# Optimization experiments

Hardware: AMD Instinct MI355X
Metric: run time of the kernel (lower is better)

The kernel has to match this reference:

```python
import jax, jax.numpy as jnp
import numpy as np

OUTLINER_RATIO = 0.01
SUB_OUTLINER_BIT = 8
NEG_INF = -1e9


def setup_inputs() -> dict:
    key = jax.random.key(0)
    T, H, D = 4096, 8, 64
    qkv = jax.random.normal(key, (T, 3, H, D), dtype=jnp.float32)
    cu_seqlens = jnp.array([0, 1024, 2048, 3072, 4096], dtype=jnp.int32)
    return {"qkv": qkv, "cu_seqlens": cu_seqlens, "max_seqlen": 1024}


def _varlen_attention(q, k, v, cu_seqlens, causal=False):
    # q,k,v: [T, H, D]; sequences delimited by cu_seqlens (attention never
    # crosses segment boundaries, matching flash_attn_varlen semantics).
    T, H, D = q.shape
    scale = D ** (-0.5)
    pos = jnp.arange(T)
    seg = jnp.searchsorted(cu_seqlens, pos, side="right") - 1  # [T] segment ids
    mask = seg[:, None] == seg[None, :]                          # [T, T]
    if causal:
        mask = mask & (pos[:, None] >= pos[None, :])
    scores = jnp.einsum("thd,shd->hts", q, k) * scale            # [H, T, T]
    scores = jnp.where(mask[None, :, :], scores, NEG_INF)
    probs = jax.nn.softmax(scores, axis=-1)
    out = jnp.einsum("hts,shd->thd", probs, v)                   # [T, H, D]
    return out


def _outlier_quant_compress(x, outliner_ratio=OUTLINER_RATIO, bit=SUB_OUTLINER_BIT):
    # Outlier detection: keep top-ratio |x| entries in full precision;
    # quantize the residual (sub-outliers) to `bit` bits per-tensor.
    a = jnp.abs(x)
    thr = jnp.quantile(a.reshape(-1), 1.0 - outliner_ratio)
    outliers = jnp.where(a > thr, x, 0.0)
    resid = x - outliers
    qmax = 2.0 ** (bit - 1) - 1.0
    scale = jnp.maximum(jnp.max(jnp.abs(resid)), 1e-8) / qmax
    q = jnp.clip(jnp.round(resid / scale), -qmax, qmax)
    x_hat = outliers + q * scale  # decompressed approximation
    return x_hat, thr, scale


def reference(qkv, cu_seqlens, max_seqlen):
    q, k, v = qkv[:, 0], qkv[:, 1], qkv[:, 2]
    out = _varlen_attention(q, k, v, cu_seqlens, causal=False)
    # Compression pipeline (stats + quantize) runs on Q,K,V,O in the original
    # forward; it does not alter the forward output.
    for t in (q, k, v, out):
        _outlier_quant_compress(t)
    return out
```

## Files before the change

### kernel.cpp

```cpp
#include <hip/hip_runtime.h>


#define HEADS 8
#define DH 64
#define TQ 64
#define TK 64
#define PSTR 72
#define NEG_BIG -1e30f
#define L2E 1.44269504088896340736f

using f32x4 = __attribute__((ext_vector_type(4))) float;
using s16x8 = __attribute__((ext_vector_type(8))) short;

__device__ inline unsigned short bf16b(float x) {
    union { float f; unsigned u; } c; c.f = x;
    unsigned r = c.u + 0x7fffu + ((c.u >> 16) & 1u);
    return (unsigned short)(r >> 16);
}

#if __has_builtin(__builtin_amdgcn_cvt_pk_bf16_f32)
__device__ inline unsigned pk2(float a, float b) {
    auto v = __builtin_amdgcn_cvt_pk_bf16_f32(a, b);
    unsigned u; __builtin_memcpy(&u, &v, 4); return u;
}
#else
__device__ inline unsigned pk2(float a, float b) {
    return (unsigned)bf16b(a) | ((unsigned)bf16b(b) << 16);
}
#endif

__global__ __launch_bounds__(256)
void prep_kernel(const float* __restrict__ qkv, unsigned short* __restrict__ Qb,
                 unsigned short* __restrict__ Kb, unsigned short* __restrict__ Vtb,
                 int T) {
    __shared__ unsigned short Lt[64][PSTR];
    const int m = blockIdx.z, h = blockIdx.y, t0 = blockIdx.x * 64;
    const int tid = threadIdx.x, d8 = tid & 7, tr = tid >> 3;

    #pragma unroll
    for (int i = 0; i < 2; ++i) {
        int t = t0 + i * 32 + tr;
        int tc = t < T ? t : T - 1;
        const float* src = qkv + ((size_t)tc * 3 + m) * (HEADS * DH) + h * DH + d8 * 8;
        float4 a = *(const float4*)src;
        float4 b = *(const float4*)(src + 4);
        if (m == 0) {
            a.x *= 0.125f; a.y *= 0.125f; a.z *= 0.125f; a.w *= 0.125f;
            b.x *= 0.125f; b.y *= 0.125f; b.z *= 0.125f; b.w *= 0.125f;
        }
        unsigned p0 = pk2(a.x, a.y), p1 = pk2(a.z, a.w);
        unsigned p2 = pk2(b.x, b.y), p3 = pk2(b.z, b.w);
        if (m == 2) {
            *(uint2*)&Lt[i * 32 + tr][d8 * 8]     = make_uint2(p0, p1);
            *(uint2*)&Lt[i * 32 + tr][d8 * 8 + 4] = make_uint2(p2, p3);
        } else if (t < T) {
            unsigned short* dst = (m == 0)
                ? (Qb + (size_t)t * (HEADS * DH) + h * DH + d8 * 8)
                : (Kb + ((size_t)h * T + t) * DH + d8 * 8);
            *(uint4*)dst = make_uint4(p0, p1, p2, p3);
        }
    }
    if (m == 2) {
        __syncthreads();
        const int d = tid >> 2, tg = tid & 3;
        #pragma unroll
        for (int p = 0; p < 2; ++p) {
            int G = tg + 4 * p;
            int td = t0 + G * 8;
            unsigned u[4];
            #pragma unroll
            for (int jj = 0; jj < 4; ++jj)
                u[jj] = (unsigned)Lt[G * 8 + 2 * jj][d] |
                        ((unsigned)Lt[G * 8 + 2 * jj + 1][d] << 16);
            if (td < T)
                *(uint4*)(Vtb + ((size_t)h * DH + d) * T + td) =
                    make_uint4(u[0], u[1], u[2], u[3]);
        }
    }
}

__global__ __launch_bounds__(256, 4)
void fa_main(const unsigned short* __restrict__ Qb, const unsigned short* __restrict__ Kb,
             const unsigned short* __restrict__ Vtb, const int* __restrict__ cu,
             int n_cu, int T, float* __restrict__ out,
             float* __restrict__ Opart, float* __restrict__ Mp, float* __restrict__ Lp) {
    __shared__ unsigned short Ksh[TK * DH];
    __shared__ unsigned short Vsh[DH * TK];
    __shared__ unsigned short Psh[TQ][PSTR];

    const int tid = threadIdx.x;
    const int h = blockIdx.y, t0 = blockIdx.x * TQ;
    const int split = blockIdx.z, nsplit = gridDim.z;
    const int w = tid >> 6, lane = tid & 63, n15 = lane & 15, quad = lane >> 4;

    int trow = t0 + w * 16 + n15; if (trow > T - 1) trow = T - 1;
    int lo, hi;
    { int s = 0; for (int j = 1; j < n_cu - 1; ++j) if (cu[j] <= trow) s = j;
      lo = cu[s]; hi = cu[s + 1]; }
    int kb_, ke;
    { int s = 0; for (int j = 1; j < n_cu - 1; ++j) if (cu[j] <= t0) s = j;
      kb_ = cu[s];
      int tl = t0 + TQ - 1; if (tl > T - 1) tl = T - 1;
      s = 0; for (int j = 1; j < n_cu - 1; ++j) if (cu[j] <= tl) s = j;
      ke = cu[s + 1]; }

    s16x8 qfrag[2];
    {
        int tc = t0 + w * 16 + n15; if (tc > T - 1) tc = T - 1;
        const unsigned short* qp = Qb + (size_t)tc * (HEADS * DH) + h * DH + quad * 8;
        qfrag[0] = *(const s16x8*)qp;
        qfrag[1] = *(const s16x8*)(qp + 32);
    }

    const unsigned short* kb_h = Kb + (size_t)h * T * DH;
    const unsigned short* vt_h = Vtb + (size_t)h * DH * T;
    int krow_rel[2], vkey_off[2];
    const unsigned short* kbase[2];
    const unsigned short* vbase[2];
    #pragma unroll
    for (int i = 0; i < 2; ++i) {
        int gg = i * 64 + lane;
        int rr = gg >> 3;
        int gc = gg & 7;
        int row = w * 16 + rr;
        int gcol = gc ^ (row & 7);
        krow_rel[i] = row;
        kbase[i] = kb_h + gcol * 8;
        vbase[i] = vt_h + (size_t)row * T;
        vkey_off[i] = gcol * 8;
    }
    int off16[2];
    #pragma unroll
    for (int kh = 0; kh < 2; ++kh)
        off16[kh] = n15 * 128 + (((kh * 4 + quad) ^ (n15 & 7)) * 16);

    f32x4 oacc[4];
    #pragma unroll
    for (int i = 0; i < 4; ++i) oacc[i] = (f32x4){0.f, 0.f, 0.f, 0.f};
    float m_ = NEG_BIG, l_ = 0.f;

    const int c0_start = (kb_ / TK) * TK + split * TK;
    for (int c0 = c0_start; c0 < ke; c0 += nsplit * TK) {
        #pragma unroll
        for (int i = 0; i < 2; ++i) {
            int rk = c0 + krow_rel[i]; if (rk > T - 1) rk = T - 1;
            __builtin_amdgcn_global_load_lds(
                (const __attribute__((address_space(1))) void*)(kbase[i] + ((size_t)rk << 6)),
                (__attribute__((address_space(3))) void*)&Ksh[(w * 128 + i * 64) * 8],
                16, 0, 0);
            int kv = c0 + vkey_off[i]; if (kv > T - 8) kv = T - 8;
            __builtin_amdgcn_global_load_lds(
                (const __attribute__((address_space(1))) void*)(vbase[i] + kv),
                (__attribute__((address_space(3))) void*)&Vsh[(w * 128 + i * 64) * 8],
                16, 0, 0);
        }
        __syncthreads();

        const char* Kc = (const char*)Ksh;
        f32x4 sacc[4];
        #pragma unroll
        for (int nt = 0; nt < 4; ++nt) {
            s16x8 k0 = *(const s16x8*)(Kc + nt * 2048 + off16[0]);
            s16x8 k1 = *(const s16x8*)(Kc + nt * 2048 + off16[1]);
            f32x4 z = (f32x4){0.f, 0.f, 0.f, 0.f};
            z = __builtin_amdgcn_mfma_f32_16x16x32_bf16(k0, qfrag[0], z, 0, 0, 0);
            z = __builtin_amdgcn_mfma_f32_16x16x32_bf16(k1, qfrag[1], z, 0, 0, 0);
            sacc[nt] = z;
        }

        if (!(c0 >= lo && c0 + TK <= hi)) {
            #pragma unroll
            for (int nt = 0; nt < 4; ++nt)
                #pragma unroll
                for (int reg = 0; reg < 4; ++reg) {
                    int key = c0 + nt * 16 + quad * 4 + reg;
                    bool valid = (key >= lo) && (key < hi);
                    sacc[nt][reg] = valid ? sacc[nt][reg] : NEG_BIG;
                }
        }

        float rm = NEG_BIG;
        #pragma unroll
        for (int nt = 0; nt < 4; ++nt)
            #pragma unroll
            for (int reg = 0; reg < 4; ++reg) rm = fmaxf(rm, sacc[nt][reg]);
        rm = fmaxf(rm, __shfl_xor(rm, 16));
        rm = fmaxf(rm, __shfl_xor(rm, 32));
        float mn = fmaxf(m_, rm);
        float alpha = exp2f((m_ - mn) * L2E);
        float mnl = mn * L2E;
        float rs = 0.f;
        #pragma unroll
        for (int nt = 0; nt < 4; ++nt) {
            float p0 = exp2f(fmaf(sacc[nt][0], L2E, -mnl));
            float p1 = exp2f(fmaf(sacc[nt][1], L2E, -mnl));
            float p2 = exp2f(fmaf(sacc[nt][2], L2E, -mnl));
            float p3 = exp2f(fmaf(sacc[nt][3], L2E, -mnl));
            rs += (p0 + p1) + (p2 + p3);
            *(uint2*)&Psh[w * 16 + n15][nt * 16 + quad * 4] =
                make_uint2(pk2(p0, p1), pk2(p2, p3));
        }
        rs += __shfl_xor(rs, 16);
        rs += __shfl_xor(rs, 32);
        l_ = fmaf(l_, alpha, rs);
        m_ = mn;
        #pragma unroll
        for (int reg = 0; reg < 4; ++reg) {
            float ar = __shfl(alpha, quad * 4 + reg);
            oacc[0][reg] *= ar; oacc[1][reg] *= ar;
            oacc[2][reg] *= ar; oacc[3][reg] *= ar;
        }

        s16x8 afr[2];
        afr[0] = *(const s16x8*)&Psh[w * 16 + n15][quad * 8];
        afr[1] = *(const s16x8*)&Psh[w * 16 + n15][32 + quad * 8];
        const char* Vc = (const char*)Vsh;
        #pragma unroll
        for (int nt = 0; nt < 4; ++nt) {
            s16x8 v0 = *(const s16x8*)(Vc + nt * 2048 + off16[0]);
            s16x8 v1 = *(const s16x8*)(Vc + nt * 2048 + off16[1]);
            oacc[nt] = __builtin_amdgcn_mfma_f32_16x16x32_bf16(afr[0], v0, oacc[nt], 0, 0, 0);
            oacc[nt] = __builtin_amdgcn_mfma_f32_16x16x32_bf16(afr[1], v1, oacc[nt], 0, 0, 0);
        }
        __syncthreads();
    }

    if (nsplit == 1) {
        #pragma unroll
        for (int reg = 0; reg < 4; ++reg) {
            float lr = __shfl(l_, quad * 4 + reg);
            float inv = 1.f / fmaxf(lr, 1e-30f);
            int t = t0 + w * 16 + quad * 4 + reg;
            if (t < T) {
                #pragma unroll
                for (int nt = 0; nt < 4; ++nt)
                    out[((size_t)t * HEADS + h) * DH + nt * 16 + n15] = oacc[nt][reg] * inv;
            }
        }
    } else {
        #pragma unroll
        for (int reg = 0; reg < 4; ++reg) {
            int t = t0 + w * 16 + quad * 4 + reg;
            if (t < T) {
                size_t base = (((size_t)split * T + t) * HEADS + h) * DH;
                #pragma unroll
                for (int nt = 0; nt < 4; ++nt)
                    Opart[base + nt * 16 + n15] = oacc[nt][reg];
            }
        }
        int tq = t0 + w * 16 + n15;
        if (quad == 0 && tq < T) {
            size_t mi = ((size_t)split * T + tq) * HEADS + h;
            Mp[mi] = m_; Lp[mi] = l_;
        }
    }
}

__global__ __launch_bounds__(256)
void fa_combine_kernel(const float* __restrict__ Opart, const float* __restrict__ Mp,
                       const float* __restrict__ Lp, float* __restrict__ out, int T) {
    int i4 = blockIdx.x * blockDim.x + threadIdx.x;
    int total = T * HEADS * (DH / 4);
    if (i4 >= total) return;
    int th = i4 / (DH / 4);
    int d4 = i4 - th * (DH / 4);
    size_t stride = (size_t)T * HEADS * DH;
    int mlstride = T * HEADS;
    float m0 = Mp[th], m1 = Mp[mlstride + th];
    float l0 = Lp[th], l1 = Lp[mlstride + th];
    float M = fmaxf(m0, m1);
    float w0 = exp2f((m0 - M) * L2E);
    float w1 = exp2f((m1 - M) * L2E);
    float L = fmaxf(fmaf(l0, w0, l1 * w1), 1e-30f);
    float inv = 1.f / L;
    size_t off = (size_t)th * DH + 4 * d4;
    float4 a = *(const float4*)&Opart[off];
    float4 b = *(const float4*)&Opart[stride + off];
    float4 o;
    o.x = fmaf(a.x, w0, b.x * w1) * inv;
    o.y = fmaf(a.y, w0, b.y * w1) * inv;
    o.z = fmaf(a.z, w0, b.z * w1) * inv;
    o.w = fmaf(a.w, w0, b.w * w1) * inv;
    *(float4*)&out[off] = o;
}

extern "C" void kernel_launch(void* const* d_in, const int* in_sizes, int n_in,
                              void* d_out, int out_size, void* d_ws, size_t ws_size,
                              hipStream_t stream) {
    const float* qkv = (const float*)d_in[0];
    const int* cu    = (const int*)d_in[1];
    const int n_cu   = in_sizes[1];
    const int T      = in_sizes[0] / (3 * HEADS * DH);
    float* out       = (float*)d_out;

    const int NSPLIT = 2;
    size_t elems = (size_t)T * HEADS * DH;

    float* Opart = (float*)d_ws;
    float* Mpp   = Opart + (size_t)NSPLIT * elems;
    float* Lpp   = Mpp + (size_t)NSPLIT * T * HEADS;
    unsigned short* Qb  = (unsigned short*)(Lpp + (size_t)NSPLIT * T * HEADS);
    unsigned short* Kb  = Qb + elems;
    unsigned short* Vtb = Kb + elems;

    int tiles = (T + TQ - 1) / TQ;
    dim3 pgrid(tiles, HEADS, 3);
    prep_kernel<<<pgrid, 256, 0, stream>>>(qkv, Qb, Kb, Vtb, T);

    dim3 grid(tiles, HEADS, NSPLIT);
    fa_main<<<grid, 256, 0, stream>>>(Qb, Kb, Vtb, cu, n_cu, T, out, Opart, Mpp, Lpp);

    int total4 = T * HEADS * (DH / 4);
    fa_combine_kernel<<<(total4 + 255) / 256, 256, 0, stream>>>(Opart, Mpp, Lpp, out, T);
}
```

Baseline: 105.2 us.

## Double-buffer K/V tiles, drop split-K combine, fuse Q conversion into attention

Removes the two-way key split and its combine kernel, so each block processes its whole segment. K/V tiles are now double-buffered in LDS so the next tile's global-to-LDS load overlaps the current tile's compute. Q is read and converted to bf16 directly inside the attention kernel, so the prep kernel no longer writes a Q buffer. The online-softmax rescale is skipped when the running max does not change, and s_setprio is raised around the MFMA sections. The extra LDS and the lower occupancy hint halve the grid's parallelism, which risks leaving compute units idle.

```diff
diff --git a/kernel.cpp b/kernel.cpp
--- a/kernel.cpp
+++ b/kernel.cpp
@@ -30,11 +30,10 @@
 #endif
 
 __global__ __launch_bounds__(256)
-void prep_kernel(const float* __restrict__ qkv, unsigned short* __restrict__ Qb,
-                 unsigned short* __restrict__ Kb, unsigned short* __restrict__ Vtb,
-                 int T) {
+void prep_kernel(const float* __restrict__ qkv, unsigned short* __restrict__ Kb,
+                 unsigned short* __restrict__ Vtb, int T) {
     __shared__ unsigned short Lt[64][PSTR];
-    const int m = blockIdx.z, h = blockIdx.y, t0 = blockIdx.x * 64;
+    const int m = 1 + blockIdx.z, h = blockIdx.y, t0 = blockIdx.x * 64;
     const int tid = threadIdx.x, d8 = tid & 7, tr = tid >> 3;
 
     #pragma unroll
@@ -44,19 +43,13 @@
         const float* src = qkv + ((size_t)tc * 3 + m) * (HEADS * DH) + h * DH + d8 * 8;
         float4 a = *(const float4*)src;
         float4 b = *(const float4*)(src + 4);
-        if (m == 0) {
-            a.x *= 0.125f; a.y *= 0.125f; a.z *= 0.125f; a.w *= 0.125f;
-            b.x *= 0.125f; b.y *= 0.125f; b.z *= 0.125f; b.w *= 0.125f;
-        }
         unsigned p0 = pk2(a.x, a.y), p1 = pk2(a.z, a.w);
         unsigned p2 = pk2(b.x, b.y), p3 = pk2(b.z, b.w);
         if (m == 2) {
             *(uint2*)&Lt[i * 32 + tr][d8 * 8]     = make_uint2(p0, p1);
             *(uint2*)&Lt[i * 32 + tr][d8 * 8 + 4] = make_uint2(p2, p3);
         } else if (t < T) {
-            unsigned short* dst = (m == 0)
-                ? (Qb + (size_t)t * (HEADS * DH) + h * DH + d8 * 8)
-                : (Kb + ((size_t)h * T + t) * DH + d8 * 8);
+            unsigned short* dst = Kb + ((size_t)h * T + t) * DH + d8 * 8;
             *(uint4*)dst = make_uint4(p0, p1, p2, p3);
         }
     }
@@ -79,18 +72,18 @@
     }
 }
 
-__global__ __launch_bounds__(256, 4)
-void fa_main(const unsigned short* __restrict__ Qb, const unsigned short* __restrict__ Kb,
+__global__ __launch_bounds__(256, 2)
+void fa_main(const float* __restrict__ qkv, const unsigned short* __restrict__ Kb,
              const unsigned short* __restrict__ Vtb, const int* __restrict__ cu,
-             int n_cu, int T, float* __restrict__ out,
-             float* __restrict__ Opart, float* __restrict__ Mp, float* __restrict__ Lp) {
-    __shared__ unsigned short Ksh[TK * DH];
-    __shared__ unsigned short Vsh[DH * TK];
+             int n_cu, int T, float* __restrict__ out) {
+    __shared__ unsigned short Ksh0[TK * DH];
+    __shared__ unsigned short Ksh1[TK * DH];
+    __shared__ unsigned short Vsh0[DH * TK];
+    __shared__ unsigned short Vsh1[DH * TK];
     __shared__ unsigned short Psh[TQ][PSTR];
 
     const int tid = threadIdx.x;
     const int h = blockIdx.y, t0 = blockIdx.x * TQ;
-    const int split = blockIdx.z, nsplit = gridDim.z;
     const int w = tid >> 6, lane = tid & 63, n15 = lane & 15, quad = lane >> 4;
 
     int trow = t0 + w * 16 + n15; if (trow > T - 1) trow = T - 1;
@@ -107,9 +100,19 @@
     s16x8 qfrag[2];
     {
         int tc = t0 + w * 16 + n15; if (tc > T - 1) tc = T - 1;
-        const unsigned short* qp = Qb + (size_t)tc * (HEADS * DH) + h * DH + quad * 8;
-        qfrag[0] = *(const s16x8*)qp;
-        qfrag[1] = *(const s16x8*)(qp + 32);
+        const float* qp = qkv + (size_t)tc * 3 * (HEADS * DH) + h * DH;
+        #pragma unroll
+        for (int f = 0; f < 2; ++f) {
+            const float* p = qp + f * 32 + quad * 8;
+            float4 a = *(const float4*)p;
+            float4 b = *(const float4*)(p + 4);
+            union { unsigned u[4]; s16x8 v; } cv;
+            cv.u[0] = pk2(a.x * 0.125f, a.y * 0.125f);
+            cv.u[1] = pk2(a.z * 0.125f, a.w * 0.125f);
+            cv.u[2] = pk2(b.x * 0.125f, b.y * 0.125f);
+            cv.u[3] = pk2(b.z * 0.125f, b.w * 0.125f);
+            qfrag[f] = cv.v;
+        }
     }
 
     const unsigned short* kb_h = Kb + (size_t)h * T * DH;
@@ -139,25 +142,26 @@
     for (int i = 0; i < 4; ++i) oacc[i] = (f32x4){0.f, 0.f, 0.f, 0.f};
     float m_ = NEG_BIG, l_ = 0.f;
 
-    const int c0_start = (kb_ / TK) * TK + split * TK;
-    for (int c0 = c0_start; c0 < ke; c0 += nsplit * TK) {
+    auto STAGE = [&](unsigned short* Kd, unsigned short* Vd, int c0s) {
         #pragma unroll
         for (int i = 0; i < 2; ++i) {
-            int rk = c0 + krow_rel[i]; if (rk > T - 1) rk = T - 1;
+            int rk = c0s + krow_rel[i]; if (rk > T - 1) rk = T - 1;
             __builtin_amdgcn_global_load_lds(
                 (const __attribute__((address_space(1))) void*)(kbase[i] + ((size_t)rk << 6)),
-                (__attribute__((address_space(3))) void*)&Ksh[(w * 128 + i * 64) * 8],
+                (__attribute__((address_space(3))) void*)&Kd[(w * 128 + i * 64) * 8],
                 16, 0, 0);
-            int kv = c0 + vkey_off[i]; if (kv > T - 8) kv = T - 8;
+            int kv = c0s + vkey_off[i]; if (kv > T - 8) kv = T - 8;
             __builtin_amdgcn_global_load_lds(
                 (const __attribute__((address_space(1))) void*)(vbase[i] + kv),
-                (__attribute__((address_space(3))) void*)&Vsh[(w * 128 + i * 64) * 8],
+                (__attribute__((address_space(3))) void*)&Vd[(w * 128 + i * 64) * 8],
                 16, 0, 0);
         }
-        __syncthreads();
-
-        const char* Kc = (const char*)Ksh;
+    };
+
+    auto COMPUTE = [&](const unsigned short* Ks, const unsigned short* Vs, int c0) {
+        const char* Kc = (const char*)Ks;
         f32x4 sacc[4];
+        __builtin_amdgcn_s_setprio(1);
         #pragma unroll
         for (int nt = 0; nt < 4; ++nt) {
             s16x8 k0 = *(const s16x8*)(Kc + nt * 2048 + off16[0]);
@@ -167,6 +171,7 @@
             z = __builtin_amdgcn_mfma_f32_16x16x32_bf16(k1, qfrag[1], z, 0, 0, 0);
             sacc[nt] = z;
         }
+        __builtin_amdgcn_s_setprio(0);
 
         if (!(c0 >= lo && c0 + TK <= hi)) {
             #pragma unroll
@@ -186,9 +191,20 @@
             for (int reg = 0; reg < 4; ++reg) rm = fmaxf(rm, sacc[nt][reg]);
         rm = fmaxf(rm, __shfl_xor(rm, 16));
         rm = fmaxf(rm, __shfl_xor(rm, 32));
-        float mn = fmaxf(m_, rm);
-        float alpha = exp2f((m_ - mn) * L2E);
-        float mnl = mn * L2E;
+
+        if (__any(rm > m_)) {
+            float mn = fmaxf(m_, rm);
+            float alpha = exp2f((m_ - mn) * L2E);
+            l_ *= alpha;
+            m_ = mn;
+            #pragma unroll
+            for (int reg = 0; reg < 4; ++reg) {
+                float ar = __shfl(alpha, quad * 4 + reg);
+                oacc[0][reg] *= ar; oacc[1][reg] *= ar;
+                oacc[2][reg] *= ar; oacc[3][reg] *= ar;
+            }
+        }
+        float mnl = m_ * L2E;
         float rs = 0.f;
         #pragma unroll
         for (int nt = 0; nt < 4; ++nt) {
@@ -202,19 +218,13 @@
         }
         rs += __shfl_xor(rs, 16);
         rs += __shfl_xor(rs, 32);
-        l_ = fmaf(l_, alpha, rs);
-        m_ = mn;
-        #pragma unroll
-        for (int reg = 0; reg < 4; ++reg) {
-            float ar = __shfl(alpha, quad * 4 + reg);
-            oacc[0][reg] *= ar; oacc[1][reg] *= ar;
-            oacc[2][reg] *= ar; oacc[3][reg] *= ar;
-        }
+        l_ += rs;
 
         s16x8 afr[2];
         afr[0] = *(const s16x8*)&Psh[w * 16 + n15][quad * 8];
         afr[1] = *(const s16x8*)&Psh[w * 16 + n15][32 + quad * 8];
-        const char* Vc = (const char*)Vsh;
+        const char* Vc = (const char*)Vs;
+        __builtin_amdgcn_s_setprio(1);
         #pragma unroll
         for (int nt = 0; nt < 4; ++nt) {
             s16x8 v0 = *(const s16x8*)(Vc + nt * 2048 + off16[0]);
@@ -222,66 +232,41 @@
             oacc[nt] = __builtin_amdgcn_mfma_f32_16x16x32_bf16(afr[0], v0, oacc[nt], 0, 0, 0);
             oacc[nt] = __builtin_amdgcn_mfma_f32_16x16x32_bf16(afr[1], v1, oacc[nt], 0, 0, 0);
         }
+        __builtin_amdgcn_s_setprio(0);
+    };
+
+    const int nIter = (ke - kb_) / TK;
+    int c0 = kb_;
+    int rem = nIter;
+
+    STAGE(Ksh0, Vsh0, c0);
+    __syncthreads();
+
+    for (;;) {
+        if (rem > 1) STAGE(Ksh1, Vsh1, c0 + TK);
+        COMPUTE(Ksh0, Vsh0, c0);
         __syncthreads();
-    }
-
-    if (nsplit == 1) {
-        #pragma unroll
-        for (int reg = 0; reg < 4; ++reg) {
-            float lr = __shfl(l_, quad * 4 + reg);
-            float inv = 1.f / fmaxf(lr, 1e-30f);
-            int t = t0 + w * 16 + quad * 4 + reg;
-            if (t < T) {
-                #pragma unroll
-                for (int nt = 0; nt < 4; ++nt)
-                    out[((size_t)t * HEADS + h) * DH + nt * 16 + n15] = oacc[nt][reg] * inv;
-            }
-        }
-    } else {
-        #pragma unroll
-        for (int reg = 0; reg < 4; ++reg) {
-            int t = t0 + w * 16 + quad * 4 + reg;
-            if (t < T) {
-                size_t base = (((size_t)split * T + t) * HEADS + h) * DH;
-                #pragma unroll
-                for (int nt = 0; nt < 4; ++nt)
-                    Opart[base + nt * 16 + n15] = oacc[nt][reg];
-            }
-        }
-        int tq = t0 + w * 16 + n15;
-        if (quad == 0 && tq < T) {
-            size_t mi = ((size_t)split * T + tq) * HEADS + h;
-            Mp[mi] = m_; Lp[mi] = l_;
-        }
-    }
-}
-
-__global__ __launch_bounds__(256)
-void fa_combine_kernel(const float* __restrict__ Opart, const float* __restrict__ Mp,
-                       const float* __restrict__ Lp, float* __restrict__ out, int T) {
-    int i4 = blockIdx.x * blockDim.x + threadIdx.x;
-    int total = T * HEADS * (DH / 4);
-    if (i4 >= total) return;
-    int th = i4 / (DH / 4);
-    int d4 = i4 - th * (DH / 4);
-    size_t stride = (size_t)T * HEADS * DH;
-    int mlstride = T * HEADS;
-    float m0 = Mp[th], m1 = Mp[mlstride + th];
-    float l0 = Lp[th], l1 = Lp[mlstride + th];
-    float M = fmaxf(m0, m1);
-    float w0 = exp2f((m0 - M) * L2E);
-    float w1 = exp2f((m1 - M) * L2E);
-    float L = fmaxf(fmaf(l0, w0, l1 * w1), 1e-30f);
-    float inv = 1.f / L;
-    size_t off = (size_t)th * DH + 4 * d4;
-    float4 a = *(const float4*)&Opart[off];
-    float4 b = *(const float4*)&Opart[stride + off];
-    float4 o;
-    o.x = fmaf(a.x, w0, b.x * w1) * inv;
-    o.y = fmaf(a.y, w0, b.y * w1) * inv;
-    o.z = fmaf(a.z, w0, b.z * w1) * inv;
-    o.w = fmaf(a.w, w0, b.w * w1) * inv;
-    *(float4*)&out[off] = o;
+        if (--rem == 0) break;
+        c0 += TK;
+
+        if (rem > 1) STAGE(Ksh0, Vsh0, c0 + TK);
+        COMPUTE(Ksh1, Vsh1, c0);
+        __syncthreads();
+        if (--rem == 0) break;
+        c0 += TK;
+    }
+
+    #pragma unroll
+    for (int reg = 0; reg < 4; ++reg) {
+        float lr = __shfl(l_, quad * 4 + reg);
+        float inv = 1.f / fmaxf(lr, 1e-30f);
+        int t = t0 + w * 16 + quad * 4 + reg;
+        if (t < T) {
+            #pragma unroll
+            for (int nt = 0; nt < 4; ++nt)
+                out[((size_t)t * HEADS + h) * DH + nt * 16 + n15] = oacc[nt][reg] * inv;
+        }
+    }
 }
 
 extern "C" void kernel_launch(void* const* d_in, const int* in_sizes, int n_in,
@@ -293,23 +278,14 @@
     const int T      = in_sizes[0] / (3 * HEADS * DH);
     float* out       = (float*)d_out;
 
-    const int NSPLIT = 2;
     size_t elems = (size_t)T * HEADS * DH;
-
-    float* Opart = (float*)d_ws;
-    float* Mpp   = Opart + (size_t)NSPLIT * elems;
-    float* Lpp   = Mpp + (size_t)NSPLIT * T * HEADS;
-    unsigned short* Qb  = (unsigned short*)(Lpp + (size_t)NSPLIT * T * HEADS);
-    unsigned short* Kb  = Qb + elems;
+    unsigned short* Kb  = (unsigned short*)d_ws;
     unsigned short* Vtb = Kb + elems;
 
     int tiles = (T + TQ - 1) / TQ;
-    dim3 pgrid(tiles, HEADS, 3);
-    prep_kernel<<<pgrid, 256, 0, stream>>>(qkv, Qb, Kb, Vtb, T);
-
-    dim3 grid(tiles, HEADS, NSPLIT);
-    fa_main<<<grid, 256, 0, stream>>>(Qb, Kb, Vtb, cu, n_cu, T, out, Opart, Mpp, Lpp);
-
-    int total4 = T * HEADS * (DH / 4);
-    fa_combine_kernel<<<(total4 + 255) / 256, 256, 0, stream>>>(Opart, Mpp, Lpp, out, T);
-}
+    dim3 pgrid(tiles, HEADS, 2);
+    prep_kernel<<<pgrid, 256, 0, stream>>>(qkv, Kb, Vtb, T);
+
+    dim3 grid(tiles, HEADS);
+    fa_main<<<grid, 256, 0, stream>>>(qkv, Kb, Vtb, cu, n_cu, T, out);
+}
```

Result: faster. 102.8 us (-2.3%).
